# Kernel tuning notes

Hardware: AMD Instinct MI355X
Metric: run time of the kernel (lower is better)

Reference implementation:

```python
import jax, jax.numpy as jnp
import numpy as np

EPS = 1e-8
V_LAMBDA = 1.0
T_LAMBDA = 1.0
BB, DIM = 8192, 256


def _rowwise_cos(a, b):
    # torch.cosine_similarity semantics: dot / (max(|a|,eps) * max(|b|,eps))
    na = jnp.maximum(jnp.linalg.norm(a, axis=-1), EPS)
    nb = jnp.maximum(jnp.linalg.norm(b, axis=-1), EPS)
    return jnp.sum(a * b, axis=-1) / (na * nb)


def _clamped_normalize(x):
    n = jnp.maximum(jnp.linalg.norm(x, axis=-1, keepdims=True), EPS)
    return x / n


def _retrieval_acc(sim, labels):
    # sim: [v, t]; top-1 retrieval accuracy in percent
    return jnp.mean((jnp.argmax(sim, axis=-1) == labels).astype(jnp.float32)) * 100.0


def setup_inputs() -> dict:
    key = jax.random.key(0)
    ks = jax.random.split(key, 5)
    names = ['vis_pred', 'text_pred', 'vis_feats_proj', 'caption_emb', 'vis_feats_proj_narr']
    return {n: jax.random.normal(k, (BB, DIM), dtype=jnp.float32) for n, k in zip(names, ks)}


def reference(vis_pred, text_pred, vis_feats_proj, caption_emb, vis_feats_proj_narr):
    bb = vis_pred.shape[0]
    labels = jnp.arange(bb)

    # training losses (row-wise cosine similarity)
    vis_loss = jnp.mean(1.0 - _rowwise_cos(vis_pred, vis_feats_proj))
    text_loss = jnp.mean(1.0 - _rowwise_cos(text_pred, caption_emb))
    loss = V_LAMBDA * vis_loss + T_LAMBDA * text_loss

    # retrieval accuracies (no_grad block). The torch repeat_interleave/repeat +
    # elementwise cosine construction is exactly the pairwise cosine-sim matrix:
    # normalize rows once, then a [bb, dim] x [dim, bb] GEMM.
    v = _clamped_normalize(jax.lax.stop_gradient(vis_pred))
    gt_v = _clamped_normalize(jax.lax.stop_gradient(vis_feats_proj))
    narr_v = _clamped_normalize(jax.lax.stop_gradient(vis_feats_proj_narr))
    gt_t = _clamped_normalize(jax.lax.stop_gradient(caption_emb))
    # NOTE: in the original code both t_r and gt_t_r are tiles of gt_text, so
    # the 'text' side of every sim matrix is gt_t. We reproduce that faithfully.

    acc_gtv_gtt = _retrieval_acc(jnp.einsum('vd,td->vt', gt_v, gt_t), labels)
    acc_v_gtt = _retrieval_acc(jnp.einsum('vd,td->vt', v, gt_t), labels)
    acc_gtv_t = _retrieval_acc(jnp.einsum('vd,td->vt', gt_v, gt_t), labels)
    acc_v_t = _retrieval_acc(jnp.einsum('vd,td->vt', v, gt_t), labels)
    acc_narr_gtt = _retrieval_acc(jnp.einsum('vd,td->vt', narr_v, gt_t), labels)
    acc_narr_t = _retrieval_acc(jnp.einsum('vd,td->vt', narr_v, gt_t), labels)

    # order: vis_loss, text_loss, loss, gt_v-gt_t, v-gt_t, gt_v-t, v-t, narr_v-gt_t, narr_v-t
    return jnp.stack([vis_loss, text_loss, loss,
                      acc_gtv_gtt, acc_v_gtt, acc_gtv_t, acc_v_t,
                      acc_narr_gtt, acc_narr_t])
```

## Files before the change

kernel.cpp:

```cpp
#include <hip/hip_runtime.h>
#include <hip/hip_bf16.h>
#include <stdint.h>
#include <limits.h>

#define BB 8192
#define DIM 256

typedef __attribute__((ext_vector_type(4))) int int32x4;

__device__ __forceinline__ void load_lds16(const char* g, char* l) {
  __builtin_amdgcn_global_load_lds(
      (const __attribute__((address_space(1))) unsigned int*)g,
      (__attribute__((address_space(3))) unsigned int*)l, 16, 0, 0);
}

__device__ __forceinline__ float q8f(float x) {
  return rintf(fmaxf(fminf(x * 256.f, 127.f), -127.f));
}

__device__ __forceinline__ int imax(int a, int b) { return a > b ? a : b; }

__device__ __forceinline__ int dpp_max16(int u) {
  int t;
  t = __builtin_amdgcn_update_dpp(0, u, 0xB1, 0xF, 0xF, true);
  u = t > u ? t : u;
  t = __builtin_amdgcn_update_dpp(0, u, 0x4E, 0xF, 0xF, true);
  u = t > u ? t : u;
  t = __builtin_amdgcn_update_dpp(0, u, 0x124, 0xF, 0xF, true);
  u = t > u ? t : u;
  t = __builtin_amdgcn_update_dpp(0, u, 0x128, 0xF, 0xF, true);
  u = t > u ? t : u;
  return u;
}

__global__ __launch_bounds__(256) void phase1(
    const float* __restrict__ vp,  const float* __restrict__ tp,
    const float* __restrict__ vfp, const float* __restrict__ ce,
    const float* __restrict__ nr,
    float* __restrict__ rowcos, int* __restrict__ diag,
    char* __restrict__ abuf,
    char* __restrict__ gtbuf,
    int* __restrict__ maxComb, float* __restrict__ sums,
    int* __restrict__ ticket) {
  __shared__ unsigned ldsT[3][4][64];
  const int wave = threadIdx.x >> 6;
  const int lane = threadIdx.x & 63;
  const int row  = blockIdx.x * 4 + wave;
  const int base = row * DIM + lane * 4;

  float4 a = *(const float4*)&vp[base];
  float4 t = *(const float4*)&tp[base];
  float4 g = *(const float4*)&vfp[base];
  float4 c = *(const float4*)&ce[base];
  float4 n = *(const float4*)&nr[base];

  float s[7];
  s[0] = a.x*a.x + a.y*a.y + a.z*a.z + a.w*a.w;
  s[1] = g.x*g.x + g.y*g.y + g.z*g.z + g.w*g.w;
  s[2] = a.x*g.x + a.y*g.y + a.z*g.z + a.w*g.w;
  s[3] = t.x*t.x + t.y*t.y + t.z*t.z + t.w*t.w;
  s[4] = c.x*c.x + c.y*c.y + c.z*c.z + c.w*c.w;
  s[5] = t.x*c.x + t.y*c.y + t.z*c.z + t.w*c.w;
  s[6] = n.x*n.x + n.y*n.y + n.z*n.z + n.w*n.w;

  #pragma unroll
  for (int mk = 1; mk < 64; mk <<= 1) {
    #pragma unroll
    for (int q = 0; q < 7; ++q) s[q] += __shfl_xor(s[q], mk);
  }

  const float eps = 1e-8f;
  float na = fmaxf(sqrtf(s[0]), eps);
  float ng = fmaxf(sqrtf(s[1]), eps);
  float nt = fmaxf(sqrtf(s[3]), eps);
  float nc = fmaxf(sqrtf(s[4]), eps);
  float nn = fmaxf(sqrtf(s[6]), eps);
  float ia = 1.f / na, ig = 1.f / ng, ic = 1.f / nc, in_ = 1.f / nn;

  float qa0=q8f(a.x*ia), qa1=q8f(a.y*ia), qa2=q8f(a.z*ia), qa3=q8f(a.w*ia);
  float qg0=q8f(g.x*ig), qg1=q8f(g.y*ig), qg2=q8f(g.z*ig), qg3=q8f(g.w*ig);
  float qn0=q8f(n.x*in_),qn1=q8f(n.y*in_),qn2=q8f(n.z*in_),qn3=q8f(n.w*in_);
  float qc0=q8f(c.x*ic), qc1=q8f(c.y*ic), qc2=q8f(c.z*ic), qc3=q8f(c.w*ic);

  float d[3];
  d[0] = qg0*qc0 + qg1*qc1 + qg2*qc2 + qg3*qc3;
  d[1] = qa0*qc0 + qa1*qc1 + qa2*qc2 + qa3*qc3;
  d[2] = qn0*qc0 + qn1*qc1 + qn2*qc2 + qn3*qc3;
  #pragma unroll
  for (int mk = 1; mk < 64; mk <<= 1) {
    #pragma unroll
    for (int q = 0; q < 3; ++q) d[q] += __shfl_xor(d[q], mk);
  }

  auto pack = [](float x0, float x1, float x2, float x3) -> unsigned {
    return ((unsigned)((int)x0 & 0xFF)) | ((unsigned)((int)x1 & 0xFF) << 8) |
           ((unsigned)((int)x2 & 0xFF) << 16) | ((unsigned)((int)x3 & 0xFF) << 24);
  };
  ((unsigned*)gtbuf)[row * 64 + lane] = pack(qc0, qc1, qc2, qc3);
  ldsT[0][wave][lane] = pack(qg0, qg1, qg2, qg3);
  ldsT[1][wave][lane] = pack(qa0, qa1, qa2, qa3);
  ldsT[2][wave][lane] = pack(qn0, qn1, qn2, qn3);

  if (lane == 0) {
    rowcos[row]        = s[2] / (na * ng);
    rowcos[BB + row]   = s[5] / (nt * nc);
    diag[0 * BB + row] = (int)d[0];
    diag[1 * BB + row] = (int)d[1];
    diag[2 * BB + row] = (int)d[2];
    maxComb[0 * BB + row] = INT_MIN;
    maxComb[1 * BB + row] = INT_MIN;
    maxComb[2 * BB + row] = INT_MIN;
  }
  if (blockIdx.x == 0 && threadIdx.x < 5) sums[threadIdx.x] = 0.f;
  if (blockIdx.x == 0 && threadIdx.x == 5) *ticket = 0;

  __syncthreads();
  if (threadIdx.x < 192) {
    int mat = threadIdx.x >> 6, l = threadIdx.x & 63;
    int kc = l >> 2, j = l & 3;
    uint4 val = *(const uint4*)&ldsT[mat][j][kc * 4];
    int tileR = blockIdx.x >> 2;
    int rm    = (blockIdx.x & 3) * 4 + j;
    *(uint4*)&abuf[(size_t)mat * BB * DIM + tileR * 4096 + kc * 256 + rm * 16] = val;
  }
}

__global__ __launch_bounds__(256, 4) void sim_argmax(
    const char* __restrict__ Af, const char* __restrict__ B,
    int* __restrict__ maxComb) {
  __shared__ char Bs[128 * 256];
  __shared__ int comb[128][2];

  const int tid  = threadIdx.x;
  const int lane = tid & 63;
  const int wave = tid >> 6;
  const int wr   = wave >> 1, wc = wave & 1;
  const int m    = lane & 15, quad = lane >> 4;
  const int z    = blockIdx.z;

  const int rowTile = blockIdx.y * 128;
  const int colTile = blockIdx.x * 128;
  const char* Az = Af + (size_t)z * BB * DIM + (size_t)(rowTile >> 4) * 4096;
  const char* Bp = B + (size_t)colTile * DIM;

  #pragma unroll
  for (int t = 0; t < 8; ++t) {
    const int c   = t * 256 + tid;
    const int row = c >> 4;
    const int l   = (c & 15) ^ (row & 15);
    load_lds16(&Bp[row * DIM + l * 16], &Bs[c * 16]);
  }

  int32x4 acc[4][4];
  #pragma unroll
  for (int i = 0; i < 4; ++i)
    #pragma unroll
    for (int j = 0; j < 4; ++j) acc[i][j] = (int32x4){0, 0, 0, 0};

  int32x4 af[4];
  #pragma unroll
  for (int rt = 0; rt < 4; ++rt)
    af[rt] = *(const int32x4*)&Az[(size_t)(wr * 4 + rt) * 4096 + lane * 16];

  __syncthreads();

  #pragma unroll
  for (int kp = 0; kp < 4; ++kp) {
    int32x4 a[4];
    #pragma unroll
    for (int rt = 0; rt < 4; ++rt) a[rt] = af[rt];
    if (kp < 3) {
      #pragma unroll
      for (int rt = 0; rt < 4; ++rt)
        af[rt] = *(const int32x4*)&Az[(size_t)(wr * 4 + rt) * 4096 +
                                      (kp + 1) * 1024 + lane * 16];
    }
    int32x4 bf[4];
    #pragma unroll
    for (int ct = 0; ct < 4; ++ct) {
      int br = wc * 64 + ct * 16 + m;
      int p  = (kp * 4 + quad) ^ m;
      bf[ct] = *(const int32x4*)&Bs[br * 256 + p * 16];
    }
    #pragma unroll
    for (int rt = 0; rt < 4; ++rt)
      #pragma unroll
      for (int ct = 0; ct < 4; ++ct)
        acc[rt][ct] = __builtin_amdgcn_mfma_i32_16x16x64_i8(
            a[rt], bf[ct], acc[rt][ct], 0, 0, 0);
  }

  const int rowBase = rowTile + wr * 64;
  const int colBase = colTile + wc * 64;
  if (blockIdx.x != blockIdx.y) {
    const int addOne = (blockIdx.y > blockIdx.x) ? 1 : 0;
    #pragma unroll
    for (int rt = 0; rt < 4; ++rt) {
      #pragma unroll
      for (int reg = 0; reg < 4; ++reg) {
        int u = imax(imax(acc[rt][0][reg], acc[rt][1][reg]),
                     imax(acc[rt][2][reg], acc[rt][3][reg]));
        u = dpp_max16(u);
        if (m == 0)
          comb[wr * 64 + rt * 16 + quad * 4 + reg][wc] = u * 2 + addOne;
      }
    }
  } else {
    #pragma unroll
    for (int rt = 0; rt < 4; ++rt) {
      #pragma unroll
      for (int reg = 0; reg < 4; ++reg) {
        int i = rowBase + rt * 16 + quad * 4 + reg;
        int u = INT_MIN;
        #pragma unroll
        for (int ct = 0; ct < 4; ++ct) {
          int j = colBase + ct * 16 + m;
          int w = acc[rt][ct][reg] * 2 + ((j < i) ? 1 : 0);
          w = (j == i) ? INT_MIN : w;
          u = imax(u, w);
        }
        u = dpp_max16(u);
        if (m == 0) comb[wr * 64 + rt * 16 + quad * 4 + reg][wc] = u;
      }
    }
  }
  __syncthreads();
  if (tid < 128) {
    int u0 = comb[tid][0], u1 = comb[tid][1];
    atomicMax(&maxComb[(size_t)z * BB + rowTile + tid], imax(u0, u1));
  }
}

__global__ __launch_bounds__(256) void phase3_fin(
    const int* __restrict__ diag, const int* __restrict__ maxComb,
    const float* __restrict__ rowcos,
    float* __restrict__ sums, int* __restrict__ ticket,
    float* __restrict__ out) {
  __shared__ float red[4][5];
  __shared__ bool amLast;
  int r = blockIdx.x * 256 + threadIdx.x;
  int lane = threadIdx.x & 63, wave = threadIdx.x >> 6;
  float v[5];
  v[0] = rowcos[r];
  v[1] = rowcos[BB + r];
  #pragma unroll
  for (int z = 0; z < 3; ++z)
    v[2 + z] = (2 * diag[z * BB + r] >= maxComb[z * BB + r]) ? 1.f : 0.f;
  #pragma unroll
  for (int mk = 1; mk < 64; mk <<= 1) {
    #pragma unroll
    for (int q = 0; q < 5; ++q) v[q] += __shfl_xor(v[q], mk);
  }
  if (lane == 0) {
    #pragma unroll
    for (int q = 0; q < 5; ++q) red[wave][q] = v[q];
  }
  __syncthreads();
  if (threadIdx.x < 5) {
    float acc = red[0][threadIdx.x] + red[1][threadIdx.x] +
                red[2][threadIdx.x] + red[3][threadIdx.x];
    atomicAdd(&sums[threadIdx.x], acc);
  }
  __threadfence();
  __syncthreads();
  if (threadIdx.x == 0)
    amLast = (atomicAdd(ticket, 1) == (int)gridDim.x - 1);
  __syncthreads();
  if (amLast && threadIdx.x == 0) {
    float s0 = atomicAdd(&sums[0], 0.f);
    float s1 = atomicAdd(&sums[1], 0.f);
    float s2 = atomicAdd(&sums[2], 0.f);
    float s3 = atomicAdd(&sums[3], 0.f);
    float s4 = atomicAdd(&sums[4], 0.f);
    float vl = 1.f - s0 * (1.f / BB);
    float tl = 1.f - s1 * (1.f / BB);
    out[0] = vl;
    out[1] = tl;
    out[2] = vl + tl;
    float a0 = s2 * (100.f / BB);
    float a1 = s3 * (100.f / BB);
    float a2 = s4 * (100.f / BB);
    out[3] = a0;
    out[4] = a1;
    out[5] = a0;
    out[6] = a1;
    out[7] = a2;
    out[8] = a2;
  }
}

extern "C" void kernel_launch(void* const* d_in, const int* in_sizes, int n_in,
                              void* d_out, int out_size, void* d_ws, size_t ws_size,
                              hipStream_t stream) {
  const float* vp  = (const float*)d_in[0];
  const float* tp  = (const float*)d_in[1];
  const float* vfp = (const float*)d_in[2];
  const float* ce  = (const float*)d_in[3];
  const float* nr  = (const float*)d_in[4];

  char* ws = (char*)d_ws;
  float* sums    = (float*)ws;
  int*   ticket  = (int*)(ws + 32);
  int*   maxComb = (int*)(ws + 64);
  int*   diag    = maxComb + 3 * BB;
  float* rowcos  = (float*)(diag + 3 * BB);
  char*  abuf    = (char*)(rowcos + 2 * BB);
  char*  gtbuf   = abuf + (size_t)3 * BB * DIM;


  phase1<<<BB / 4, 256, 0, stream>>>(vp, tp, vfp, ce, nr, rowcos, diag,
                                     abuf, gtbuf, maxComb, sums, ticket);

  dim3 grid(BB / 128, BB / 128, 3);
  sim_argmax<<<grid, 256, 0, stream>>>(abuf, gtbuf, maxComb);

  phase3_fin<<<BB / 256, 256, 0, stream>>>(diag, maxComb, rowcos, sums, ticket,
                                           (float*)d_out);
}
```

Measured before the change: 152.6 us.

## Widen sim tile to 256 cols and loop all three A matrices per block

The sim_argmax kernel now loads a 128x256 B tile into LDS once and reuses it across all three query matrices (z loop inside the block), instead of launching one grid slice per matrix with a 128x128 tile. Each wave computes a 64x128 sub-tile with double-buffered A register prefetch across z and k steps. The LDS comb reduction is replaced by direct per-row atomicMax from each wave. This cuts redundant B global/LDS traffic and the block count, but doubles LDS and accumulator registers, lowering occupancy (launch bounds 4→2) and doubling the atomic count.

```diff
diff --git a/kernel.cpp b/kernel.cpp
--- a/kernel.cpp
+++ b/kernel.cpp
@@ -125,109 +125,108 @@
   }
 }
 
-__global__ __launch_bounds__(256, 4) void sim_argmax(
+__global__ __launch_bounds__(256, 2) void sim_argmax(
     const char* __restrict__ Af, const char* __restrict__ B,
     int* __restrict__ maxComb) {
-  __shared__ char Bs[128 * 256];
-  __shared__ int comb[128][2];
+  __shared__ char Bs[256 * 256];
 
   const int tid  = threadIdx.x;
   const int lane = tid & 63;
   const int wave = tid >> 6;
   const int wr   = wave >> 1, wc = wave & 1;
   const int m    = lane & 15, quad = lane >> 4;
-  const int z    = blockIdx.z;
 
   const int rowTile = blockIdx.y * 128;
-  const int colTile = blockIdx.x * 128;
-  const char* Az = Af + (size_t)z * BB * DIM + (size_t)(rowTile >> 4) * 4096;
+  const int colTile = blockIdx.x * 256;
   const char* Bp = B + (size_t)colTile * DIM;
 
   #pragma unroll
-  for (int t = 0; t < 8; ++t) {
+  for (int t = 0; t < 16; ++t) {
     const int c   = t * 256 + tid;
     const int row = c >> 4;
     const int l   = (c & 15) ^ (row & 15);
     load_lds16(&Bp[row * DIM + l * 16], &Bs[c * 16]);
   }
 
-  int32x4 acc[4][4];
-  #pragma unroll
-  for (int i = 0; i < 4; ++i)
-    #pragma unroll
-    for (int j = 0; j < 4; ++j) acc[i][j] = (int32x4){0, 0, 0, 0};
-
-  int32x4 af[4];
+  const char* A0 = Af + ((size_t)(rowTile >> 4) + wr * 4) * 4096;
+
+  int32x4 af[2][4];
   #pragma unroll
   for (int rt = 0; rt < 4; ++rt)
-    af[rt] = *(const int32x4*)&Az[(size_t)(wr * 4 + rt) * 4096 + lane * 16];
-
-  __syncthreads();
-
-  #pragma unroll
-  for (int kp = 0; kp < 4; ++kp) {
-    int32x4 a[4];
-    #pragma unroll
-    for (int rt = 0; rt < 4; ++rt) a[rt] = af[rt];
-    if (kp < 3) {
+    af[0][rt] = *(const int32x4*)&A0[(size_t)rt * 4096 + lane * 16];
+
+  __syncthreads();
+
+  const int rowBase  = rowTile + wr * 64;
+  const int colStrip = colTile + wc * 128;
+  const int32x4 zero = (int32x4){0, 0, 0, 0};
+
+  int32x4 acc[4][8];
+
+  #pragma unroll
+  for (int z = 0; z < 3; ++z) {
+    #pragma unroll
+    for (int kp = 0; kp < 4; ++kp) {
+      const int pb = (z * 4 + kp) & 1;
+      if (!(z == 2 && kp == 3)) {
+        const int zn = (kp < 3) ? z : z + 1;
+        const int kn = (kp < 3) ? kp + 1 : 0;
+        const char* An = A0 + (size_t)zn * BB * DIM;
+        #pragma unroll
+        for (int rt = 0; rt < 4; ++rt)
+          af[pb ^ 1][rt] =
+              *(const int32x4*)&An[(size_t)rt * 4096 + kn * 1024 + lane * 16];
+      }
+      int32x4 bf[8];
+      #pragma unroll
+      for (int ct = 0; ct < 8; ++ct) {
+        int br = wc * 128 + ct * 16 + m;
+        int p  = (kp * 4 + quad) ^ m;
+        bf[ct] = *(const int32x4*)&Bs[br * 256 + p * 16];
+      }
       #pragma unroll
       for (int rt = 0; rt < 4; ++rt)
-        af[rt] = *(const int32x4*)&Az[(size_t)(wr * 4 + rt) * 4096 +
-                                      (kp + 1) * 1024 + lane * 16];
+        #pragma unroll
+        for (int ct = 0; ct < 8; ++ct)
+          acc[rt][ct] = __builtin_amdgcn_mfma_i32_16x16x64_i8(
+              af[pb][rt], bf[ct], (kp == 0) ? zero : acc[rt][ct], 0, 0, 0);
     }
-    int32x4 bf[4];
-    #pragma unroll
-    for (int ct = 0; ct < 4; ++ct) {
-      int br = wc * 64 + ct * 16 + m;
-      int p  = (kp * 4 + quad) ^ m;
-      bf[ct] = *(const int32x4*)&Bs[br * 256 + p * 16];
-    }
-    #pragma unroll
-    for (int rt = 0; rt < 4; ++rt)
+
+    int* mz = maxComb + (size_t)z * BB;
+    if (rowTile != colStrip) {
+      const int addOne = (rowTile > colStrip) ? 1 : 0;
       #pragma unroll
-      for (int ct = 0; ct < 4; ++ct)
-        acc[rt][ct] = __builtin_amdgcn_mfma_i32_16x16x64_i8(
-            a[rt], bf[ct], acc[rt][ct], 0, 0, 0);
-  }
-
-  const int rowBase = rowTile + wr * 64;
-  const int colBase = colTile + wc * 64;
-  if (blockIdx.x != blockIdx.y) {
-    const int addOne = (blockIdx.y > blockIdx.x) ? 1 : 0;
-    #pragma unroll
-    for (int rt = 0; rt < 4; ++rt) {
+      for (int rt = 0; rt < 4; ++rt) {
+        #pragma unroll
+        for (int reg = 0; reg < 4; ++reg) {
+          int u = imax(imax(imax(acc[rt][0][reg], acc[rt][1][reg]),
+                            imax(acc[rt][2][reg], acc[rt][3][reg])),
+                       imax(imax(acc[rt][4][reg], acc[rt][5][reg]),
+                            imax(acc[rt][6][reg], acc[rt][7][reg])));
+          u = dpp_max16(u);
+          if (m == 0)
+            atomicMax(&mz[rowBase + rt * 16 + quad * 4 + reg], u * 2 + addOne);
+        }
+      }
+    } else {
       #pragma unroll
-      for (int reg = 0; reg < 4; ++reg) {
-        int u = imax(imax(acc[rt][0][reg], acc[rt][1][reg]),
-                     imax(acc[rt][2][reg], acc[rt][3][reg]));
-        u = dpp_max16(u);
-        if (m == 0)
-          comb[wr * 64 + rt * 16 + quad * 4 + reg][wc] = u * 2 + addOne;
+      for (int rt = 0; rt < 4; ++rt) {
+        #pragma unroll
+        for (int reg = 0; reg < 4; ++reg) {
+          const int i = rowBase + rt * 16 + quad * 4 + reg;
+          int u = INT_MIN;
+          #pragma unroll
+          for (int ct = 0; ct < 8; ++ct) {
+            const int j = colStrip + ct * 16 + m;
+            int w = acc[rt][ct][reg] * 2 + ((j < i) ? 1 : 0);
+            w = (j == i) ? INT_MIN : w;
+            u = imax(u, w);
+          }
+          u = dpp_max16(u);
+          if (m == 0) atomicMax(&mz[i], u);
+        }
       }
     }
-  } else {
-    #pragma unroll
-    for (int rt = 0; rt < 4; ++rt) {
-      #pragma unroll
-      for (int reg = 0; reg < 4; ++reg) {
-        int i = rowBase + rt * 16 + quad * 4 + reg;
-        int u = INT_MIN;
-        #pragma unroll
-        for (int ct = 0; ct < 4; ++ct) {
-          int j = colBase + ct * 16 + m;
-          int w = acc[rt][ct][reg] * 2 + ((j < i) ? 1 : 0);
-          w = (j == i) ? INT_MIN : w;
-          u = imax(u, w);
-        }
-        u = dpp_max16(u);
-        if (m == 0) comb[wr * 64 + rt * 16 + quad * 4 + reg][wc] = u;
-      }
-    }
-  }
-  __syncthreads();
-  if (tid < 128) {
-    int u0 = comb[tid][0], u1 = comb[tid][1];
-    atomicMax(&maxComb[(size_t)z * BB + rowTile + tid], imax(u0, u1));
   }
 }
 
@@ -311,7 +310,7 @@
   phase1<<<BB / 4, 256, 0, stream>>>(vp, tp, vfp, ce, nr, rowcos, diag,
                                      abuf, gtbuf, maxComb, sums, ticket);
 
-  dim3 grid(BB / 128, BB / 128, 3);
+  dim3 grid(BB / 256, BB / 128);
   sim_argmax<<<grid, 256, 0, stream>>>(abuf, gtbuf, maxComb);
 
   phase3_fin<<<BB / 256, 256, 0, stream>>>(diag, maxComb, rowcos, sums, ticket,
```

Result: slower. 180.7 us (+18.4%).
